# Performance work log

Measured on AMD Instinct MI355X. Metric: run time of the kernel, lower is better.

## Reference

```python
import jax, jax.numpy as jnp
import numpy as np

VAR0, VAR1 = 0.1, 0.2
THRESHOLD = 0.35
NEGPOS_RATIO = 7
LOW_GT_THRESH = 0.2  # match() filters GT whose best prior IoU < 0.2


def setup_inputs() -> dict:
    key = jax.random.key(0)
    ks = jax.random.split(key, 8)
    B, P, G = 16, 43008, 128
    loc_data = jax.random.normal(ks[0], (B, P, 4), jnp.float32)
    conf_data = jax.random.normal(ks[1], (B, P, 2), jnp.float32)
    landm_data = jax.random.normal(ks[2], (B, P, 10), jnp.float32)
    # priors in cxcywh form, positive sizes
    pc = jax.random.uniform(ks[3], (P, 2), jnp.float32)
    pwh = jax.random.uniform(ks[4], (P, 2), jnp.float32, minval=0.02, maxval=0.32)
    priors = jnp.concatenate([pc, pwh], axis=1)
    # targets: valid xyxy boxes + 10 landmark coords + label (face=1)
    ctr = jax.random.uniform(ks[5], (B, G, 2), jnp.float32, minval=0.2, maxval=0.8)
    wh = jax.random.uniform(ks[6], (B, G, 2), jnp.float32, minval=0.05, maxval=0.3)
    boxes = jnp.concatenate([ctr - wh / 2, ctr + wh / 2], axis=-1)
    landms = jax.random.uniform(ks[7], (B, G, 10), jnp.float32)
    labels = jnp.ones((B, G, 1), jnp.float32)
    targets = jnp.concatenate([boxes, landms, labels], axis=-1)
    return {"loc_data": loc_data, "conf_data": conf_data, "landm_data": landm_data,
            "priors": priors, "targets": targets}


def point_form(priors):
    return jnp.concatenate([priors[:, :2] - priors[:, 2:] / 2,
                            priors[:, :2] + priors[:, 2:] / 2], axis=1)


def jaccard(a, b):  # a: [G,4] xyxy, b: [P,4] xyxy -> [G,P]
    lt = jnp.maximum(a[:, None, :2], b[None, :, :2])
    rb = jnp.minimum(a[:, None, 2:], b[None, :, 2:])
    wh = jnp.clip(rb - lt, 0.0)
    inter = wh[..., 0] * wh[..., 1]
    area_a = (a[:, 2] - a[:, 0]) * (a[:, 3] - a[:, 1])
    area_b = (b[:, 2] - b[:, 0]) * (b[:, 3] - b[:, 1])
    return inter / (area_a[:, None] + area_b[None, :] - inter)


def encode(matched, priors):  # matched xyxy [P,4], priors cxcywh [P,4]
    g_cxcy = (matched[:, :2] + matched[:, 2:]) / 2 - priors[:, :2]
    g_cxcy = g_cxcy / (VAR0 * priors[:, 2:])
    g_wh = jnp.log((matched[:, 2:] - matched[:, :2]) / priors[:, 2:]) / VAR1
    return jnp.concatenate([g_cxcy, g_wh], axis=1)


def encode_landm(matched, priors):  # matched [P,10], priors [P,4]
    m = matched.reshape(-1, 5, 2)
    g = (m - priors[:, None, :2]) / (VAR0 * priors[:, None, 2:])
    return g.reshape(-1, 10)


def match_one(truths, labels, landms, priors):
    G = truths.shape[0]
    overlaps = jaccard(truths, point_form(priors))  # [G, P]
    best_prior_overlap = overlaps.max(axis=1)       # [G]
    best_prior_idx = overlaps.argmax(axis=1)        # [G]
    valid = best_prior_overlap >= LOW_GT_THRESH
    any_valid = jnp.any(valid)
    best_truth_overlap = overlaps.max(axis=0)       # [P]
    best_truth_idx = overlaps.argmax(axis=0)        # [P]
    # index_fill_(0, best_prior_idx_filter, 2): ensure each valid GT keeps its best prior
    fill_val = jnp.where(valid, 2.0, best_truth_overlap[best_prior_idx])
    best_truth_overlap = best_truth_overlap.at[best_prior_idx].set(fill_val)
    # best_truth_idx[best_prior_idx[j]] = j for all j
    best_truth_idx = best_truth_idx.at[best_prior_idx].set(jnp.arange(G))
    matches = truths[best_truth_idx]                       # [P,4]
    conf = labels[best_truth_idx].astype(jnp.int32)        # [P]
    conf = jnp.where(best_truth_overlap < THRESHOLD, 0, conf)
    conf = jnp.where(any_valid, conf, 0)  # no valid GT -> all background
    loc = encode(matches, priors)
    landm = encode_landm(landms[best_truth_idx], priors)
    return loc, conf, landm


def smooth_l1(x):
    ax = jnp.abs(x)
    return jnp.where(ax < 1.0, 0.5 * ax * ax, ax - 0.5)


def reference(loc_data, conf_data, landm_data, priors, targets):
    truths = targets[..., :4]
    landms = targets[..., 4:14]
    labels = targets[..., 14]
    loc_t, conf_t, landm_t = jax.vmap(
        lambda t, l, lm: match_one(t, l, lm, priors))(truths, labels, landms)

    # landmark loss over positives
    pos1 = conf_t > 0
    N1 = jnp.maximum(pos1.sum().astype(jnp.float32), 1.0)
    loss_landm = jnp.sum(smooth_l1(landm_data - landm_t) * pos1[..., None])

    # localization loss over positives
    pos = conf_t != 0
    num_pos = pos.sum(axis=1, keepdims=True)  # [B,1]
    loss_l = jnp.sum(smooth_l1(loc_data - loc_t) * pos[..., None])

    # hard negative mining on per-prior CE loss
    lse = jax.scipy.special.logsumexp(conf_data, axis=-1)  # [B,P]
    gathered = jnp.take_along_axis(conf_data, conf_t[..., None], axis=-1)[..., 0]
    ce_all = lse - gathered                                # [B,P] per-prior CE
    mine = jnp.where(pos, 0.0, ce_all)
    loss_idx = jnp.argsort(-mine, axis=1)
    idx_rank = jnp.argsort(loss_idx, axis=1)
    num_neg = jnp.clip(NEGPOS_RATIO * num_pos, None, pos.shape[1] - 1)
    neg = idx_rank < num_neg
    sel = pos | neg
    loss_c = jnp.sum(jnp.where(sel, ce_all, 0.0))

    N = jnp.maximum(num_pos.sum().astype(jnp.float32), 1.0)
    return loss_l / N, loss_c / N, loss_landm / N1
```

## Files before the change

### kernel.cpp

```cpp
#include <hip/hip_runtime.h>
#include <stdint.h>


#define GC 8
#define PPT 4
#define PPI 2

typedef float v2f __attribute__((ext_vector_type(2)));
__device__ __forceinline__ v2f v2max(v2f a, v2f b) {
  return __builtin_elementwise_max(a, b);
}
__device__ __forceinline__ v2f v2min(v2f a, v2f b) {
  return __builtin_elementwise_min(a, b);
}

__device__ __forceinline__ float sl1(float x) {
  float a = fabsf(x);
  return a < 1.f ? 0.5f * a * a : a - 0.5f;
}

__device__ __forceinline__ double dwave(double v) {
#pragma unroll
  for (int o = 32; o; o >>= 1) v += __shfl_down(v, o);
  return v;
}

__global__ __launch_bounds__(256) void k_match(
    const float* __restrict__ priors, const float* __restrict__ targets,
    float* __restrict__ bto, int* __restrict__ bti,
    unsigned long long* __restrict__ bp, int P, int G, int NIOU, int PT2,
    int NGC, int PC) {
  int tid = threadIdx.x;
  __shared__ float4 sgt[128];
  __shared__ unsigned long long sred[GC * 256];

  if ((int)blockIdx.x < NIOU) {
    int b = blockIdx.x / PT2, tile = blockIdx.x % PT2;
    int base = tile * (256 * PPI);
    for (int g = tid; g < G; g += 256) {
      const float* t = targets + ((size_t)b * G + g) * 15;
      sgt[g] = make_float4(t[0], t[1], t[2], t[3]);
    }
    __syncthreads();

    v2f plt[PPI], prb[PPI];
    float pa[PPI], bi[PPI], bu[PPI];
    int bidx[PPI];
#pragma unroll
    for (int k = 0; k < PPI; ++k) {
      int p = base + tid + k * 256;
      int pl = p < P ? p : P - 1;
      float4 pr = ((const float4*)priors)[pl];
      v2f c = {pr.x, pr.y}, h = {pr.z * 0.5f, pr.w * 0.5f};
      plt[k] = c - h; prb[k] = c + h;
      pa[k] = pr.z * pr.w;
      bi[k] = -1.f; bu[k] = 1.f; bidx[k] = 0;
    }
    for (int g = 0; g < G; ++g) {
      float4 T = sgt[g];
      v2f Tlt = {T.x, T.y}, Trb = {T.z, T.w};
      v2f gd = Trb - Tlt;
      float A = gd.x * gd.y;
#pragma unroll
      for (int k = 0; k < PPI; ++k) {
        v2f lt = v2max(Tlt, plt[k]);
        v2f rb = v2min(Trb, prb[k]);
        v2f d = v2max(rb - lt, (v2f)(0.f));
        float inter = d.x * d.y;
        float uni = (A + pa[k]) - inter;
        if (inter * bu[k] > bi[k] * uni) { bi[k] = inter; bu[k] = uni; bidx[k] = g; }
      }
    }
#pragma unroll
    for (int k = 0; k < PPI; ++k) {
      int p = base + tid + k * 256;
      if (p < P) {
        bto[(size_t)b * P + p] = bi[k] / bu[k];
        bti[(size_t)b * P + p] = bidx[k];
      }
    }
  } else {
    int bc = blockIdx.x - NIOU;
    int pc = bc % PC;
    int gcb = (bc / PC) % NGC;
    int b = bc / (PC * NGC);
    int g0 = gcb * GC;

    if (tid < GC) {
      int g = g0 + tid;
      float4 v = make_float4(0.f, 0.f, 0.f, 0.f);
      if (g < G) {
        const float* t = targets + ((size_t)b * G + g) * 15;
        v = make_float4(t[0], t[1], t[2], t[3]);
      }
      sgt[tid] = v;
    }
    __syncthreads();

    v2f glt[GC], grb[GC];
    float ga[GC];
#pragma unroll
    for (int j = 0; j < GC; ++j) {
      float4 T = sgt[j];
      glt[j] = (v2f){T.x, T.y};
      grb[j] = (v2f){T.z, T.w};
      ga[j] = (T.z - T.x) * (T.w - T.y);
    }

    float bi[GC], bu[GC];
    unsigned bpp[GC];
#pragma unroll
    for (int j = 0; j < GC; ++j) { bi[j] = -1.f; bu[j] = 1.f; bpp[j] = 0; }

    int chunk = (P + PC - 1) / PC;
    int ps = pc * chunk;
    int pe = ps + chunk; if (pe > P) pe = P;

    for (int p = ps + tid; p < pe; p += 256) {
      float4 pr = ((const float4*)priors)[p];
      v2f c = {pr.x, pr.y}, h = {pr.z * 0.5f, pr.w * 0.5f};
      v2f plt = c - h, prb = c + h;
      float pa = pr.z * pr.w;
#pragma unroll
      for (int j = 0; j < GC; ++j) {
        v2f lt = v2max(glt[j], plt);
        v2f rb = v2min(grb[j], prb);
        v2f d = v2max(rb - lt, (v2f)(0.f));
        float inter = d.x * d.y;
        float uni = (ga[j] + pa) - inter;
        if (inter * bu[j] > bi[j] * uni) { bi[j] = inter; bu[j] = uni; bpp[j] = (unsigned)p; }
      }
    }

#pragma unroll
    for (int j = 0; j < GC; ++j) {
      unsigned long long pk = 0ULL;
      if (bi[j] >= 0.f) {
        float iou = bi[j] / bu[j];
        pk = ((unsigned long long)__float_as_uint(iou) << 32) |
             (unsigned)(~bpp[j]);
      }
      sred[j * 256 + tid] = pk;
    }
    __syncthreads();
    {
      int j = tid >> 5, s = tid & 31;
      unsigned long long m = sred[j * 256 + s];
#pragma unroll
      for (int t = 1; t < 8; ++t) {
        unsigned long long v = sred[j * 256 + s + t * 32];
        if (v > m) m = v;
      }
      __syncthreads();
      sred[j * 256 + s] = m;
    }
    __syncthreads();
    if (tid < GC) {
      unsigned long long m = sred[tid * 256];
      for (int s = 1; s < 32; ++s) {
        unsigned long long v = sred[tid * 256 + s];
        if (v > m) m = v;
      }
      int g = g0 + tid;
      if (g < G && m) atomicMax(&bp[(size_t)b * G + g], m);
    }
  }
}

__global__ void k_scatter(const unsigned long long* __restrict__ bp,
                          float* __restrict__ bto, int* __restrict__ bti,
                          int* __restrict__ anyv, int P, int G) {
  int b = blockIdx.x, g = threadIdx.x;
  __shared__ unsigned spp[128];
  __shared__ int s_any;
  if (g == 0) s_any = 0;
  __syncthreads();
  unsigned long long m = bp[(size_t)b * G + g];
  unsigned pp = ~(unsigned)m;
  float val = __uint_as_float((unsigned)(m >> 32));
  bool ok = (m != 0ULL);
  float oldv = 0.f;
  if (ok) oldv = bto[(size_t)b * P + pp];
  spp[g] = ok ? pp : 0xFFFFFFFFu;
  if (ok && val >= 0.2f) s_any = 1;
  __syncthreads();
  bool win = ok;
  for (int g2 = g + 1; g2 < G; ++g2)
    if (spp[g2] == pp) win = false;
  if (win) {
    bto[(size_t)b * P + pp] = (val >= 0.2f) ? 2.0f : oldv;
    bti[(size_t)b * P + pp] = g;
  }
  __syncthreads();
  if (g == 0) anyv[b] = s_any;
}

__global__ __launch_bounds__(256) void k_main(
    const float* __restrict__ loc, const float* __restrict__ conf,
    const float* __restrict__ lm, const float* __restrict__ priors,
    const float* __restrict__ targets, const float* __restrict__ bto,
    const int* __restrict__ bti, const int* __restrict__ anyv,
    float* __restrict__ mine, unsigned* __restrict__ h1,
    double* __restrict__ pll, double* __restrict__ pllm,
    double* __restrict__ plc, int* __restrict__ pnp, int P, int G, int PT) {
  int b = blockIdx.x / PT, tile = blockIdx.x % PT;
  int tid = threadIdx.x;
  int p = tile * 256 + tid;

  __shared__ float st[128 * 15];
  __shared__ unsigned hist[1024];
  __shared__ double rs[12];
  __shared__ int ri[4];

  for (int i = tid; i < G * 15; i += 256) st[i] = targets[(size_t)b * G * 15 + i];
  for (int i = tid; i < 1024; i += 256) hist[i] = 0;
  __syncthreads();

  double ll = 0, llm = 0, lc = 0;
  int np = 0;
  if (p < P) {
    size_t idx = (size_t)b * P + p;
    int av = anyv[b];
    float ov = bto[idx];
    int ti = bti[idx];
    bool pos = av && (ov >= 0.35f);

    float2 c = ((const float2*)conf)[idx];
    float mx = fmaxf(c.x, c.y);
    float lse = mx + logf(expf(c.x - mx) + expf(c.y - mx));
    float ce = lse - (pos ? c.y : c.x);
    float mv = pos ? 0.f : ce;
    mine[idx] = mv;
    atomicAdd(&hist[__float_as_uint(mv) >> 21], 1u);

    if (pos) {
      np = 1;
      lc = (double)ce;
      float4 pr = ((const float4*)priors)[p];
      const float* t = st + ti * 15;
      float dx = 0.1f * pr.z, dy = 0.1f * pr.w;
      float gx = ((t[0] + t[2]) * 0.5f - pr.x) / dx;
      float gy = ((t[1] + t[3]) * 0.5f - pr.y) / dy;
      float gw = logf((t[2] - t[0]) / pr.z) * 5.0f;
      float gh = logf((t[3] - t[1]) / pr.w) * 5.0f;
      float4 ld = ((const float4*)loc)[idx];
      ll = (double)(sl1(ld.x - gx) + sl1(ld.y - gy) + sl1(ld.z - gw) +
                    sl1(ld.w - gh));
      const float2* lmd = (const float2*)lm + idx * 5;
      float s = 0.f;
#pragma unroll
      for (int j = 0; j < 5; ++j) {
        float2 lv = lmd[j];
        float ex = (t[4 + 2 * j] - pr.x) / dx;
        float ey = (t[5 + 2 * j] - pr.y) / dy;
        s += sl1(lv.x - ex) + sl1(lv.y - ey);
      }
      llm = (double)s;
    }
  }

  ll = dwave(ll);
  llm = dwave(llm);
  lc = dwave(lc);
#pragma unroll
  for (int o = 32; o; o >>= 1) np += __shfl_down(np, o);
  int lane = tid & 63, wid = tid >> 6;
  if (lane == 0) { rs[wid] = ll; rs[4 + wid] = llm; rs[8 + wid] = lc; ri[wid] = np; }
  __syncthreads();
  if (tid == 0) {
    pll[blockIdx.x] = rs[0] + rs[1] + rs[2] + rs[3];
    pllm[blockIdx.x] = rs[4] + rs[5] + rs[6] + rs[7];
    plc[blockIdx.x] = rs[8] + rs[9] + rs[10] + rs[11];
    pnp[blockIdx.x] = ri[0] + ri[1] + ri[2] + ri[3];
  }
  for (int i = tid; i < 1024; i += 256)
    if (hist[i]) atomicAdd(&h1[(size_t)b * 1024 + i], hist[i]);
}

__global__ __launch_bounds__(256) void k_sel1(const unsigned* __restrict__ h1,
                                              const int* __restrict__ pnp,
                                              int* __restrict__ num_pos, int P,
                                              int PT, int* __restrict__ pfx1,
                                              int* __restrict__ k1) {
  int b = blockIdx.x, tid = threadIdx.x;
  __shared__ int sn[256];
  int n = 0;
  for (int i = tid; i < PT; i += 256) n += pnp[b * PT + i];
  sn[tid] = n;
  __syncthreads();
  for (int off = 128; off; off >>= 1) {
    if (tid < off) sn[tid] += sn[tid + off];
    __syncthreads();
  }
  int npos = sn[0];
  if (tid == 0) num_pos[b] = npos;

  const unsigned* h = h1 + (size_t)b * 1024;
  __shared__ unsigned S[256];
  unsigned p0 = h[tid * 4], p1 = h[tid * 4 + 1], p2 = h[tid * 4 + 2],
           p3 = h[tid * 4 + 3];
  S[tid] = p0 + p1 + p2 + p3;
  __syncthreads();
  for (int off = 1; off < 256; off <<= 1) {
    unsigned add = (tid + off < 256) ? S[tid + off] : 0;
    __syncthreads();
    S[tid] += add;
    __syncthreads();
  }
  long long k = 7LL * (long long)npos;
  long long cap = P - 1;
  if (k > cap) k = cap;
  int cnt = __syncthreads_count(k > 0 && (long long)S[tid] >= k);
  if (cnt == 0) {
    if (tid == 0) { pfx1[b] = -1; k1[b] = 0; }
    return;
  }
  int seg = cnt - 1;
  if (tid == seg) {
    long long cum = (seg + 1 < 256) ? (long long)S[seg + 1] : 0;
    unsigned hv[4] = {p0, p1, p2, p3};
    int bin = seg * 4;
    for (int j = 3; j >= 0; --j) {
      if (cum + hv[j] >= k) { bin = seg * 4 + j; break; }
      cum += hv[j];
    }
    pfx1[b] = bin;
    k1[b] = (int)(k - cum);
  }
}

__global__ __launch_bounds__(256) void k_h2(const float* __restrict__ mine,
                                            const int* __restrict__ pfx1,
                                            unsigned* __restrict__ h2, int P,
                                            int PT4) {
  int b = blockIdx.x / PT4;
  int base = (blockIdx.x % PT4) * (256 * PPT) + threadIdx.x;
  __shared__ unsigned hist[2048];
  for (int i = threadIdx.x; i < 2048; i += 256) hist[i] = 0;
  __syncthreads();
  int pf = pfx1[b];
#pragma unroll
  for (int k = 0; k < PPT; ++k) {
    int p = base + k * 256;
    if (p < P) {
      unsigned bits = __float_as_uint(mine[(size_t)b * P + p]);
      if ((int)(bits >> 21) == pf) atomicAdd(&hist[(bits >> 10) & 2047], 1u);
    }
  }
  __syncthreads();
  for (int i = threadIdx.x; i < 2048; i += 256)
    if (hist[i]) atomicAdd(&h2[(size_t)b * 2048 + i], hist[i]);
}

__global__ __launch_bounds__(256) void k_sel2(const unsigned* __restrict__ h2,
                                              const int* __restrict__ pfx1,
                                              const int* __restrict__ k1,
                                              int* __restrict__ pfx21,
                                              int* __restrict__ k2) {
  int b = blockIdx.x, tid = threadIdx.x;
  const unsigned* h = h2 + (size_t)b * 2048;
  __shared__ unsigned S[256];
  unsigned hv[8];
  unsigned s = 0;
#pragma unroll
  for (int j = 0; j < 8; ++j) { hv[j] = h[tid * 8 + j]; s += hv[j]; }
  S[tid] = s;
  __syncthreads();
  for (int off = 1; off < 256; off <<= 1) {
    unsigned add = (tid + off < 256) ? S[tid + off] : 0;
    __syncthreads();
    S[tid] += add;
    __syncthreads();
  }
  int pf = pfx1[b];
  long long k = (long long)k1[b];
  int cnt = __syncthreads_count(pf >= 0 && (long long)S[tid] >= k);
  if (cnt == 0) {
    if (tid == 0) { pfx21[b] = -1; k2[b] = 0; }
    return;
  }
  int seg = cnt - 1;
  if (tid == seg) {
    long long cum = (seg + 1 < 256) ? (long long)S[seg + 1] : 0;
    int bin = seg * 8;
    for (int j = 7; j >= 0; --j) {
      if (cum + hv[j] >= k) { bin = seg * 8 + j; break; }
      cum += hv[j];
    }
    pfx21[b] = (pf << 11) | bin;
    k2[b] = (int)(k - cum);
  }
}

__global__ __launch_bounds__(256) void k_h3(const float* __restrict__ mine,
                                            const int* __restrict__ pfx21,
                                            unsigned* __restrict__ h3, int P,
                                            int PT4) {
  int b = blockIdx.x / PT4;
  int base = (blockIdx.x % PT4) * (256 * PPT) + threadIdx.x;
  __shared__ unsigned hist[1024];
  for (int i = threadIdx.x; i < 1024; i += 256) hist[i] = 0;
  __syncthreads();
  int pf = pfx21[b];
#pragma unroll
  for (int k = 0; k < PPT; ++k) {
    int p = base + k * 256;
    if (p < P) {
      unsigned bits = __float_as_uint(mine[(size_t)b * P + p]);
      if ((int)(bits >> 10) == pf) atomicAdd(&hist[bits & 1023], 1u);
    }
  }
  __syncthreads();
  for (int i = threadIdx.x; i < 1024; i += 256)
    if (hist[i]) atomicAdd(&h3[(size_t)b * 1024 + i], hist[i]);
}

__global__ __launch_bounds__(256) void k_sel3(const unsigned* __restrict__ h3,
                                              const int* __restrict__ pfx21,
                                              const int* __restrict__ k2,
                                              int* __restrict__ tbits,
                                              double* __restrict__ tieadd) {
  int b = blockIdx.x, tid = threadIdx.x;
  const unsigned* h = h3 + (size_t)b * 1024;
  __shared__ unsigned S[256];
  unsigned p0 = h[tid * 4], p1 = h[tid * 4 + 1], p2 = h[tid * 4 + 2],
           p3 = h[tid * 4 + 3];
  S[tid] = p0 + p1 + p2 + p3;
  __syncthreads();
  for (int off = 1; off < 256; off <<= 1) {
    unsigned add = (tid + off < 256) ? S[tid + off] : 0;
    __syncthreads();
    S[tid] += add;
    __syncthreads();
  }
  int pf = pfx21[b];
  long long k = (long long)k2[b];
  int cnt = __syncthreads_count(pf >= 0 && (long long)S[tid] >= k);
  if (cnt == 0) {
    if (tid == 0) tbits[b] = -1;
    return;
  }
  int seg = cnt - 1;
  if (tid == seg) {
    long long cum = (seg + 1 < 256) ? (long long)S[seg + 1] : 0;
    unsigned hv[4] = {p0, p1, p2, p3};
    int bin = seg * 4;
    for (int j = 3; j >= 0; --j) {
      if (cum + hv[j] >= k) { bin = seg * 4 + j; break; }
      cum += hv[j];
    }
    unsigned tb = ((unsigned)pf << 10) | (unsigned)bin;
    tbits[b] = (int)tb;
    long long nat = k - cum;
    tieadd[b] = (double)nat * (double)__uint_as_float(tb);
  }
}

__global__ __launch_bounds__(256) void k_fsum(const float* __restrict__ mine,
                                              const int* __restrict__ tbits,
                                              double* __restrict__ pfs, int P,
                                              int PT4) {
  int b = blockIdx.x / PT4;
  int base = (blockIdx.x % PT4) * (256 * PPT) + threadIdx.x;
  unsigned tb = (unsigned)tbits[b];
  double v = 0.0;
#pragma unroll
  for (int k = 0; k < PPT; ++k) {
    int p = base + k * 256;
    if (p < P) {
      unsigned bits = __float_as_uint(mine[(size_t)b * P + p]);
      if (bits > tb) v += (double)__uint_as_float(bits);
    }
  }
  v = dwave(v);
  __shared__ double rs[4];
  int lane = threadIdx.x & 63, wid = threadIdx.x >> 6;
  if (lane == 0) rs[wid] = v;
  __syncthreads();
  if (threadIdx.x == 0) pfs[blockIdx.x] = rs[0] + rs[1] + rs[2] + rs[3];
}

__global__ __launch_bounds__(256) void k_fin(
    const double* __restrict__ pll, const double* __restrict__ pllm,
    const double* __restrict__ plc, const double* __restrict__ pfs,
    const double* __restrict__ tieadd, const int* __restrict__ num_pos,
    float* __restrict__ out, int NBm, int NB4, int B) {
  int tid = threadIdx.x;
  double a = 0, c = 0, d = 0, f = 0, t = 0, n = 0;
  for (int i = tid; i < NBm; i += 256) { a += pll[i]; c += pllm[i]; d += plc[i]; }
  for (int i = tid; i < NB4; i += 256) f += pfs[i];
  for (int i = tid; i < B; i += 256) { t += tieadd[i]; n += (double)num_pos[i]; }
  a = dwave(a); c = dwave(c); d = dwave(d); f = dwave(f); t = dwave(t);
  n = dwave(n);
  __shared__ double rs[6 * 4];
  int lane = tid & 63, wid = tid >> 6;
  if (lane == 0) {
    rs[wid] = a; rs[4 + wid] = c; rs[8 + wid] = d;
    rs[12 + wid] = f; rs[16 + wid] = t; rs[20 + wid] = n;
  }
  __syncthreads();
  if (tid == 0) {
    double A = rs[0] + rs[1] + rs[2] + rs[3];
    double C = rs[4] + rs[5] + rs[6] + rs[7];
    double D = rs[8] + rs[9] + rs[10] + rs[11];
    double F = rs[12] + rs[13] + rs[14] + rs[15];
    double T = rs[16] + rs[17] + rs[18] + rs[19];
    double N = rs[20] + rs[21] + rs[22] + rs[23];
    if (N < 1.0) N = 1.0;
    out[0] = (float)(A / N);
    out[1] = (float)((D + F + T) / N);
    out[2] = (float)(C / N);
  }
}

extern "C" void kernel_launch(void* const* d_in, const int* in_sizes, int n_in,
                              void* d_out, int out_size, void* d_ws,
                              size_t ws_size, hipStream_t stream) {
  const float* loc = (const float*)d_in[0];
  const float* conf = (const float*)d_in[1];
  const float* lm = (const float*)d_in[2];
  const float* priors = (const float*)d_in[3];
  const float* targets = (const float*)d_in[4];

  int P = in_sizes[3] / 4;
  int B = in_sizes[0] / (4 * P);
  int G = in_sizes[4] / (15 * B);
  int PT = (P + 255) / 256;
  int PT2 = (P + 256 * PPI - 1) / (256 * PPI);
  int PT4 = (P + 256 * PPT - 1) / (256 * PPT);
  int NBm = B * PT;
  int NB4 = B * PT4;
  int NGC = (G + GC - 1) / GC;
  int PC = 8;
  int NIOU = B * PT2;
  int NBP = B * NGC * PC;

  char* w = (char*)d_ws;
  size_t off = 0;
  unsigned long long* bp = (unsigned long long*)(w + off);
  off += (size_t)B * G * 8;
  double* tieadd = (double*)(w + off);
  off += (size_t)B * 8;
  int* ctrl = (int*)(w + off);
  off += (size_t)(8 * B) * 4;
  int* anyv = ctrl;
  int* num_pos = ctrl + B;
  int* pfx1 = ctrl + 2 * B;
  int* k1 = ctrl + 3 * B;
  int* pfx21 = ctrl + 4 * B;
  int* k2 = ctrl + 5 * B;
  int* tbits = ctrl + 6 * B;
  unsigned* h1 = (unsigned*)(w + off);
  off += (size_t)B * 1024 * 4;
  unsigned* h2 = (unsigned*)(w + off);
  off += (size_t)B * 2048 * 4;
  unsigned* h3 = (unsigned*)(w + off);
  off += (size_t)B * 1024 * 4;
  size_t clear_bytes = off;
  off = (off + 255) & ~(size_t)255;
  float* bto = (float*)(w + off);
  off += (size_t)B * P * 4;
  int* bti = (int*)(w + off);
  off += (size_t)B * P * 4;
  float* mine = (float*)(w + off);
  off += (size_t)B * P * 4;
  double* pll = (double*)(w + off);
  off += (size_t)NBm * 8;
  double* pllm = (double*)(w + off);
  off += (size_t)NBm * 8;
  double* plc = (double*)(w + off);
  off += (size_t)NBm * 8;
  double* pfs = (double*)(w + off);
  off += (size_t)NB4 * 8;
  int* pnp = (int*)(w + off);
  off += (size_t)NBm * 4;

  hipMemsetAsync(d_ws, 0, clear_bytes, stream);

  k_match<<<NIOU + NBP, 256, 0, stream>>>(priors, targets, bto, bti, bp, P, G,
                                          NIOU, PT2, NGC, PC);
  k_scatter<<<B, G, 0, stream>>>(bp, bto, bti, anyv, P, G);
  k_main<<<B * PT, 256, 0, stream>>>(loc, conf, lm, priors, targets, bto, bti,
                                     anyv, mine, h1, pll, pllm, plc, pnp, P, G,
                                     PT);
  k_sel1<<<B, 256, 0, stream>>>(h1, pnp, num_pos, P, PT, pfx1, k1);
  k_h2<<<B * PT4, 256, 0, stream>>>(mine, pfx1, h2, P, PT4);
  k_sel2<<<B, 256, 0, stream>>>(h2, pfx1, k1, pfx21, k2);
  k_h3<<<B * PT4, 256, 0, stream>>>(mine, pfx21, h3, P, PT4);
  k_sel3<<<B, 256, 0, stream>>>(h3, pfx21, k2, tbits, tieadd);
  k_fsum<<<B * PT4, 256, 0, stream>>>(mine, tbits, pfs, P, PT4);
  k_fin<<<1, 256, 0, stream>>>(pll, pllm, plc, pfs, tieadd, num_pos,
                               (float*)d_out, NBm, NB4, B);
}
```

Before: 221.3 us.

## Scalarize IoU loops, unroll two-way, and early-exit radix select when all negatives selected

Replaces packed v2f min/max with scalar fminf/fmaxf in both matching paths and processes two GTs or two priors per iteration to expose more ILP. It also adds a fast path in the selection chain: when the negative count reaches P-1, sel1 marks the batch as 'select all', and the later histogram and select kernels return early. This skips the h2/h3 passes for such batches. The best-prior reduction now starts from IoU 0 with a default index and always issues the atomicMax, which changes tie and zero-overlap handling slightly.

```diff
diff --git a/kernel.cpp b/kernel.cpp
--- a/kernel.cpp
+++ b/kernel.cpp
@@ -5,14 +5,6 @@
 #define GC 8
 #define PPT 4
 #define PPI 2
-
-typedef float v2f __attribute__((ext_vector_type(2)));
-__device__ __forceinline__ v2f v2max(v2f a, v2f b) {
-  return __builtin_elementwise_max(a, b);
-}
-__device__ __forceinline__ v2f v2min(v2f a, v2f b) {
-  return __builtin_elementwise_min(a, b);
-}
 
 __device__ __forceinline__ float sl1(float x) {
   float a = fabsf(x);
@@ -43,32 +35,43 @@
     }
     __syncthreads();
 
-    v2f plt[PPI], prb[PPI];
-    float pa[PPI], bi[PPI], bu[PPI];
+    float px1[PPI], py1[PPI], px2[PPI], py2[PPI], pa[PPI];
+    float bi[PPI], bu[PPI];
     int bidx[PPI];
 #pragma unroll
     for (int k = 0; k < PPI; ++k) {
       int p = base + tid + k * 256;
       int pl = p < P ? p : P - 1;
       float4 pr = ((const float4*)priors)[pl];
-      v2f c = {pr.x, pr.y}, h = {pr.z * 0.5f, pr.w * 0.5f};
-      plt[k] = c - h; prb[k] = c + h;
+      px1[k] = pr.x - pr.z * 0.5f; py1[k] = pr.y - pr.w * 0.5f;
+      px2[k] = pr.x + pr.z * 0.5f; py2[k] = pr.y + pr.w * 0.5f;
       pa[k] = pr.z * pr.w;
       bi[k] = -1.f; bu[k] = 1.f; bidx[k] = 0;
     }
-    for (int g = 0; g < G; ++g) {
-      float4 T = sgt[g];
-      v2f Tlt = {T.x, T.y}, Trb = {T.z, T.w};
-      v2f gd = Trb - Tlt;
-      float A = gd.x * gd.y;
+
+    for (int g = 0; g < G; g += 2) {
+      float4 T0 = sgt[g];
+      float4 T1 = sgt[g + 1];
+      float A0 = (T0.z - T0.x) * (T0.w - T0.y);
+      float A1 = (T1.z - T1.x) * (T1.w - T1.y);
 #pragma unroll
       for (int k = 0; k < PPI; ++k) {
-        v2f lt = v2max(Tlt, plt[k]);
-        v2f rb = v2min(Trb, prb[k]);
-        v2f d = v2max(rb - lt, (v2f)(0.f));
-        float inter = d.x * d.y;
-        float uni = (A + pa[k]) - inter;
-        if (inter * bu[k] > bi[k] * uni) { bi[k] = inter; bu[k] = uni; bidx[k] = g; }
+        {
+          float iw = fminf(T0.z, px2[k]) - fmaxf(T0.x, px1[k]);
+          float ih = fminf(T0.w, py2[k]) - fmaxf(T0.y, py1[k]);
+          iw = fmaxf(iw, 0.f); ih = fmaxf(ih, 0.f);
+          float inter = iw * ih;
+          float uni = (A0 + pa[k]) - inter;
+          if (inter * bu[k] > bi[k] * uni) { bi[k] = inter; bu[k] = uni; bidx[k] = g; }
+        }
+        {
+          float iw = fminf(T1.z, px2[k]) - fmaxf(T1.x, px1[k]);
+          float ih = fminf(T1.w, py2[k]) - fmaxf(T1.y, py1[k]);
+          iw = fmaxf(iw, 0.f); ih = fmaxf(ih, 0.f);
+          float inter = iw * ih;
+          float uni = (A1 + pa[k]) - inter;
+          if (inter * bu[k] > bi[k] * uni) { bi[k] = inter; bu[k] = uni; bidx[k] = g + 1; }
+        }
       }
     }
 #pragma unroll
@@ -97,49 +100,62 @@
     }
     __syncthreads();
 
-    v2f glt[GC], grb[GC];
-    float ga[GC];
+    float gx1[GC], gy1[GC], gx2[GC], gy2[GC], ga[GC];
 #pragma unroll
     for (int j = 0; j < GC; ++j) {
       float4 T = sgt[j];
-      glt[j] = (v2f){T.x, T.y};
-      grb[j] = (v2f){T.z, T.w};
+      gx1[j] = T.x; gy1[j] = T.y; gx2[j] = T.z; gy2[j] = T.w;
       ga[j] = (T.z - T.x) * (T.w - T.y);
     }
-
-    float bi[GC], bu[GC];
-    unsigned bpp[GC];
-#pragma unroll
-    for (int j = 0; j < GC; ++j) { bi[j] = -1.f; bu[j] = 1.f; bpp[j] = 0; }
 
     int chunk = (P + PC - 1) / PC;
     int ps = pc * chunk;
     int pe = ps + chunk; if (pe > P) pe = P;
-
-    for (int p = ps + tid; p < pe; p += 256) {
-      float4 pr = ((const float4*)priors)[p];
-      v2f c = {pr.x, pr.y}, h = {pr.z * 0.5f, pr.w * 0.5f};
-      v2f plt = c - h, prb = c + h;
-      float pa = pr.z * pr.w;
+    int count = pe - ps;
+
+    float bi[GC], bu[GC];
+    unsigned bpp[GC];
+#pragma unroll
+    for (int j = 0; j < GC; ++j) { bi[j] = 0.f; bu[j] = 1.f; bpp[j] = (unsigned)(ps + tid); }
+
+    for (int i = tid; i < count; i += 512) {
+      int p0 = ps + i;
+      int i1 = i + 256;
+      int p1 = (i1 < count) ? ps + i1 : p0;
+      float4 q0 = ((const float4*)priors)[p0];
+      float4 q1 = ((const float4*)priors)[p1];
+      float ax1 = q0.x - q0.z * 0.5f, ay1 = q0.y - q0.w * 0.5f;
+      float ax2 = q0.x + q0.z * 0.5f, ay2 = q0.y + q0.w * 0.5f;
+      float aa = q0.z * q0.w;
+      float bx1 = q1.x - q1.z * 0.5f, by1 = q1.y - q1.w * 0.5f;
+      float bx2 = q1.x + q1.z * 0.5f, by2 = q1.y + q1.w * 0.5f;
+      float ba = q1.z * q1.w;
 #pragma unroll
       for (int j = 0; j < GC; ++j) {
-        v2f lt = v2max(glt[j], plt);
-        v2f rb = v2min(grb[j], prb);
-        v2f d = v2max(rb - lt, (v2f)(0.f));
-        float inter = d.x * d.y;
-        float uni = (ga[j] + pa) - inter;
-        if (inter * bu[j] > bi[j] * uni) { bi[j] = inter; bu[j] = uni; bpp[j] = (unsigned)p; }
+        {
+          float iw = fminf(gx2[j], ax2) - fmaxf(gx1[j], ax1);
+          float ih = fminf(gy2[j], ay2) - fmaxf(gy1[j], ay1);
+          iw = fmaxf(iw, 0.f); ih = fmaxf(ih, 0.f);
+          float inter = iw * ih;
+          float uni = (ga[j] + aa) - inter;
+          if (inter * bu[j] > bi[j] * uni) { bi[j] = inter; bu[j] = uni; bpp[j] = (unsigned)p0; }
+        }
+        {
+          float iw = fminf(gx2[j], bx2) - fmaxf(gx1[j], bx1);
+          float ih = fminf(gy2[j], by2) - fmaxf(gy1[j], by1);
+          iw = fmaxf(iw, 0.f); ih = fmaxf(ih, 0.f);
+          float inter = iw * ih;
+          float uni = (ga[j] + ba) - inter;
+          if (inter * bu[j] > bi[j] * uni) { bi[j] = inter; bu[j] = uni; bpp[j] = (unsigned)p1; }
+        }
       }
     }
 
 #pragma unroll
     for (int j = 0; j < GC; ++j) {
-      unsigned long long pk = 0ULL;
-      if (bi[j] >= 0.f) {
-        float iou = bi[j] / bu[j];
-        pk = ((unsigned long long)__float_as_uint(iou) << 32) |
-             (unsigned)(~bpp[j]);
-      }
+      float iou = bi[j] / bu[j];
+      unsigned long long pk =
+          ((unsigned long long)__float_as_uint(iou) << 32) | (unsigned)(~bpp[j]);
       sred[j * 256 + tid] = pk;
     }
     __syncthreads();
@@ -162,7 +178,7 @@
         if (v > m) m = v;
       }
       int g = g0 + tid;
-      if (g < G && m) atomicMax(&bp[(size_t)b * G + g], m);
+      if (g < G) atomicMax(&bp[(size_t)b * G + g], m);
     }
   }
 }
@@ -281,7 +297,8 @@
                                               const int* __restrict__ pnp,
                                               int* __restrict__ num_pos, int P,
                                               int PT, int* __restrict__ pfx1,
-                                              int* __restrict__ k1) {
+                                              int* __restrict__ k1,
+                                              int* __restrict__ tbits) {
   int b = blockIdx.x, tid = threadIdx.x;
   __shared__ int sn[256];
   int n = 0;
@@ -295,6 +312,17 @@
   int npos = sn[0];
   if (tid == 0) num_pos[b] = npos;
 
+  long long k = 7LL * (long long)npos;
+  long long cap = P - 1;
+  if (k <= 0) {
+    if (tid == 0) { pfx1[b] = -1; k1[b] = 0; }
+    return;
+  }
+  if (k >= cap) {
+    if (tid == 0) { pfx1[b] = -2; k1[b] = 0; tbits[b] = 0; }
+    return;
+  }
+
   const unsigned* h = h1 + (size_t)b * 1024;
   __shared__ unsigned S[256];
   unsigned p0 = h[tid * 4], p1 = h[tid * 4 + 1], p2 = h[tid * 4 + 2],
@@ -307,10 +335,7 @@
     S[tid] += add;
     __syncthreads();
   }
-  long long k = 7LL * (long long)npos;
-  long long cap = P - 1;
-  if (k > cap) k = cap;
-  int cnt = __syncthreads_count(k > 0 && (long long)S[tid] >= k);
+  int cnt = __syncthreads_count((long long)S[tid] >= k);
   if (cnt == 0) {
     if (tid == 0) { pfx1[b] = -1; k1[b] = 0; }
     return;
@@ -334,11 +359,12 @@
                                             unsigned* __restrict__ h2, int P,
                                             int PT4) {
   int b = blockIdx.x / PT4;
+  int pf = pfx1[b];
+  if (pf < 0) return;
   int base = (blockIdx.x % PT4) * (256 * PPT) + threadIdx.x;
   __shared__ unsigned hist[2048];
   for (int i = threadIdx.x; i < 2048; i += 256) hist[i] = 0;
   __syncthreads();
-  int pf = pfx1[b];
 #pragma unroll
   for (int k = 0; k < PPT; ++k) {
     int p = base + k * 256;
@@ -358,6 +384,11 @@
                                               int* __restrict__ pfx21,
                                               int* __restrict__ k2) {
   int b = blockIdx.x, tid = threadIdx.x;
+  int pf = pfx1[b];
+  if (pf < 0) {
+    if (tid == 0) { pfx21[b] = pf; k2[b] = 0; }
+    return;
+  }
   const unsigned* h = h2 + (size_t)b * 2048;
   __shared__ unsigned S[256];
   unsigned hv[8];
@@ -372,9 +403,8 @@
     S[tid] += add;
     __syncthreads();
   }
-  int pf = pfx1[b];
   long long k = (long long)k1[b];
-  int cnt = __syncthreads_count(pf >= 0 && (long long)S[tid] >= k);
+  int cnt = __syncthreads_count((long long)S[tid] >= k);
   if (cnt == 0) {
     if (tid == 0) { pfx21[b] = -1; k2[b] = 0; }
     return;
@@ -397,11 +427,12 @@
                                             unsigned* __restrict__ h3, int P,
                                             int PT4) {
   int b = blockIdx.x / PT4;
+  int pf = pfx21[b];
+  if (pf < 0) return;
   int base = (blockIdx.x % PT4) * (256 * PPT) + threadIdx.x;
   __shared__ unsigned hist[1024];
   for (int i = threadIdx.x; i < 1024; i += 256) hist[i] = 0;
   __syncthreads();
-  int pf = pfx21[b];
 #pragma unroll
   for (int k = 0; k < PPT; ++k) {
     int p = base + k * 256;
@@ -421,6 +452,12 @@
                                               int* __restrict__ tbits,
                                               double* __restrict__ tieadd) {
   int b = blockIdx.x, tid = threadIdx.x;
+  int pf = pfx21[b];
+  if (pf == -2) return;
+  if (pf == -1) {
+    if (tid == 0) tbits[b] = -1;
+    return;
+  }
   const unsigned* h = h3 + (size_t)b * 1024;
   __shared__ unsigned S[256];
   unsigned p0 = h[tid * 4], p1 = h[tid * 4 + 1], p2 = h[tid * 4 + 2],
@@ -433,9 +470,8 @@
     S[tid] += add;
     __syncthreads();
   }
-  int pf = pfx21[b];
   long long k = (long long)k2[b];
-  int cnt = __syncthreads_count(pf >= 0 && (long long)S[tid] >= k);
+  int cnt = __syncthreads_count((long long)S[tid] >= k);
   if (cnt == 0) {
     if (tid == 0) tbits[b] = -1;
     return;
@@ -583,7 +619,7 @@
   k_main<<<B * PT, 256, 0, stream>>>(loc, conf, lm, priors, targets, bto, bti,
                                      anyv, mine, h1, pll, pllm, plc, pnp, P, G,
                                      PT);
-  k_sel1<<<B, 256, 0, stream>>>(h1, pnp, num_pos, P, PT, pfx1, k1);
+  k_sel1<<<B, 256, 0, stream>>>(h1, pnp, num_pos, P, PT, pfx1, k1, tbits);
   k_h2<<<B * PT4, 256, 0, stream>>>(mine, pfx1, h2, P, PT4);
   k_sel2<<<B, 256, 0, stream>>>(h2, pfx1, k1, pfx21, k2);
   k_h3<<<B * PT4, 256, 0, stream>>>(mine, pfx21, h3, P, PT4);
```

Result: faster. 197.8 us (-10.6%).
